# Kernel tuning notes

Hardware: AMD Instinct MI355X
Metric: run time of the kernel (lower is better)

The kernel has to match this reference:

```python
import jax, jax.numpy as jnp
import numpy as np

N0, N1, N2 = 200000, 50000, 10000   # node counts per hop (src -> layer1 targets -> layer2 targets)
E1, E2 = 1000000, 250000
C_IN, H = 128, 256


def setup_inputs() -> dict:
    key = jax.random.key(0)
    ks = jax.random.split(key, 10)
    return {
        "x": jax.random.normal(ks[0], (N0, C_IN), dtype=jnp.float32),
        "src1": jax.random.randint(ks[1], (E1,), 0, N0, dtype=jnp.int32),
        "dst1": jax.random.randint(ks[2], (E1,), 0, N1, dtype=jnp.int32),
        "src2": jax.random.randint(ks[3], (E2,), 0, N1, dtype=jnp.int32),
        "dst2": jax.random.randint(ks[4], (E2,), 0, N2, dtype=jnp.int32),
        "Wl1": jax.random.normal(ks[5], (C_IN, H), dtype=jnp.float32) / np.sqrt(C_IN),
        "Wr1": jax.random.normal(ks[6], (C_IN, H), dtype=jnp.float32) / np.sqrt(C_IN),
        "b1": jnp.zeros((H,), dtype=jnp.float32),
        "Wl2": jax.random.normal(ks[7], (H, H), dtype=jnp.float32) / np.sqrt(H),
        "Wr2": jax.random.normal(ks[8], (H, H), dtype=jnp.float32) / np.sqrt(H),
        "b2": jnp.zeros((H,), dtype=jnp.float32),
    }


def _sage_conv(x_src, x_dst, src, dst, Wl, Wr, b, n_dst):
    # mean aggregation of neighbor messages (PyG SAGEConv, aggr='mean', root_weight=True)
    msgs = x_src[src]                                             # [E, C] irregular gather
    agg = jax.ops.segment_sum(msgs, dst, num_segments=n_dst)      # [n_dst, C]
    cnt = jax.ops.segment_sum(jnp.ones_like(dst, dtype=x_src.dtype), dst, num_segments=n_dst)
    agg = agg / jnp.maximum(cnt, 1.0)[:, None]
    return agg @ Wl + x_dst @ Wr + b


def reference(x, src1, dst1, src2, dst2, Wl1, Wr1, b1, Wl2, Wr2, b2):
    # layer 1: targets are first N1 nodes
    h = _sage_conv(x, x[:N1], src1, dst1, Wl1, Wr1, b1, N1)       # [N1, H]
    h = jax.nn.relu(h)                                            # dropout: eval mode (identity)
    # layer 2: targets are first N2 nodes of the layer-1 output
    out = _sage_conv(h, h[:N2], src2, dst2, Wl2, Wr2, b2, N2)     # [N2, H]
    return out
```

## Files before the change

### kernel.cpp

```cpp
#include <hip/hip_runtime.h>

#define N0 200000
#define N1 50000
#define N2 10000
#define E1 1000000
#define E2 250000
#define CIN 128
#define HD  256

#define SH1   6
#define PK1   18
#define NB1   782
#define CAP1  2048
#define DPB1  64
#define SH2   4
#define PK2   16
#define NB2   625
#define CAP2  640
#define DPB2  16

#define NBIN1 489
#define NBIN2 123
#define NPREP 768
#define NCVT  25000

typedef __attribute__((ext_vector_type(8))) short short8;
typedef __attribute__((ext_vector_type(4))) float f32x4;

__device__ __forceinline__ unsigned short f2bf(float f) {
    unsigned u = __builtin_bit_cast(unsigned, f);
    u = (u + 0x7fffu + ((u >> 16) & 1u)) >> 16;
    return (unsigned short)u;
}
__device__ __forceinline__ float bf2f(unsigned short h) {
    unsigned u = ((unsigned)h) << 16;
    return __builtin_bit_cast(float, u);
}

template<int SHIFTB, int PACKSH, int CAP>
__device__ __forceinline__ void bin_body(
    int bb, const int* __restrict__ src, const int* __restrict__ dst,
    int* __restrict__ gcnt, unsigned* __restrict__ binned, int E, int* sh)
{
    int* hcnt  = sh;
    int* hbase = sh + 1024;
    int* hcur  = sh + 2048;
    const int t = threadIdx.x;
    #pragma unroll
    for (int j = 0; j < 4; j++) hcnt[t + j * 256] = 0;
    __syncthreads();

    unsigned pk[8];
    int      bk[8];
    const int e0 = bb * 2048;
    #pragma unroll
    for (int j = 0; j < 8; j++) {
        const int e = e0 + j * 256 + t;
        if (e < E) {
            const int d = dst[e];
            const int s = src[e];
            bk[j] = d >> SHIFTB;
            pk[j] = ((unsigned)(d & ((1 << SHIFTB) - 1)) << PACKSH) | (unsigned)s;
            atomicAdd(&hcnt[bk[j]], 1);
        } else bk[j] = -1;
    }
    __syncthreads();

    #pragma unroll
    for (int j = 0; j < 4; j++) {
        const int i = t + j * 256;
        hbase[i] = atomicAdd(&gcnt[i], hcnt[i]);
        hcur[i]  = 0;
    }
    __syncthreads();

    #pragma unroll
    for (int j = 0; j < 8; j++) {
        if (bk[j] >= 0) {
            const int idx = atomicAdd(&hcur[bk[j]], 1);
            binned[(size_t)bk[j] * CAP + hbase[bk[j]] + idx] = pk[j];
        }
    }
}

__global__ __launch_bounds__(256) void megaA_kernel(
    const float* __restrict__ x, unsigned short* __restrict__ xb,
    const float* __restrict__ Wl1, const float* __restrict__ Wr1,
    const float* __restrict__ Wl2, const float* __restrict__ Wr2,
    unsigned short* __restrict__ wsw1, unsigned short* __restrict__ wsw2,
    const int* __restrict__ src1, const int* __restrict__ dst1,
    const int* __restrict__ src2, const int* __restrict__ dst2,
    int* __restrict__ gcnt1, int* __restrict__ gcnt2,
    unsigned* __restrict__ binned1, unsigned* __restrict__ binned2)
{
    __shared__ int sh[3072];
    const int b = blockIdx.x;
    const int t = threadIdx.x;

    if (b < NBIN1) {
        bin_body<SH1, PK1, CAP1>(b, src1, dst1, gcnt1, binned1, E1, sh);
    } else if (b < NBIN1 + NBIN2) {
        bin_body<SH2, PK2, CAP2>(b - NBIN1, src2, dst2, gcnt2, binned2, E2, sh);
    } else if (b < NBIN1 + NBIN2 + NPREP) {
        const int pb = b - NBIN1 - NBIN2;
        const float* Wl; const float* Wr; unsigned short* wsw; int K, tid;
        if (pb < 256) { Wl = Wl1; Wr = Wr1; wsw = wsw1; K = CIN; tid = pb * 256 + t; }
        else          { Wl = Wl2; Wr = Wr2; wsw = wsw2; K = HD;  tid = (pb - 256) * 256 + t; }
        const int j  = tid & 7;
        const int L  = (tid >> 3) & 63;
        const int nt = (tid >> 9) & 15;
        const int kt = tid >> 13;
        const int k  = kt * 32 + (L >> 4) * 8 + j;
        const int n  = nt * 16 + (L & 15);
        const float v = (k < K) ? Wl[(size_t)k * HD + n]
                                : Wr[(size_t)(k - K) * HD + n];
        wsw[tid] = f2bf(v);
    } else {
        const int i = (b - NBIN1 - NBIN2 - NPREP) * 256 + t;
        const float4 v = ((const float4*)x)[i];
        ushort4 o;
        o.x = f2bf(v.x); o.y = f2bf(v.y); o.z = f2bf(v.z); o.w = f2bf(v.w);
        ((ushort4*)xb)[i] = o;
    }
}

__global__ __launch_bounds__(512) void layer1_mega(
    const unsigned short* __restrict__ xb,
    const unsigned* __restrict__ binned1, const int* __restrict__ gcnt1,
    const unsigned short* __restrict__ wsw1, const float* __restrict__ bias,
    unsigned short* __restrict__ hb)
{
    __shared__ int ebuf[CAP1];
    __shared__ int lhist[DPB1], loff[DPB1], lcur[DPB1];
    __shared__ __align__(16) unsigned short aggT[4 * DPB1 * 4 * 8];

    const int t = threadIdx.x;
    const int b = blockIdx.x;
    const int cnt = gcnt1[b];
    const unsigned* bp = binned1 + (size_t)b * CAP1;

    if (t < DPB1) lhist[t] = 0;
    __syncthreads();
    for (int i = t; i < cnt; i += 512)
        atomicAdd(&lhist[bp[i] >> PK1], 1);
    __syncthreads();
    const int h0 = (t < DPB1) ? lhist[t] : 0;
    __syncthreads();
    #pragma unroll
    for (int ofs = 1; ofs < DPB1; ofs <<= 1) {
        const int u = (t >= ofs && t < DPB1) ? lhist[t - ofs] : 0;
        __syncthreads();
        if (t < DPB1) lhist[t] += u;
        __syncthreads();
    }
    if (t < DPB1) { loff[t] = lhist[t] - h0; lcur[t] = lhist[t] - h0; }
    __syncthreads();
    for (int i = t; i < cnt; i += 512) {
        const unsigned p = bp[i];
        const int slot = atomicAdd(&lcur[p >> PK1], 1);
        ebuf[slot] = (int)(p & ((1u << PK1) - 1u));
    }
    __syncthreads();

    const int w = t >> 6, L = t & 63, half = L >> 5, l32 = L & 31;
    const int ktw = l32 >> 3, qw = (l32 >> 1) & 3, jo = (l32 & 1) * 4;
    for (int r = w; r < DPB1; r += 8) {
        const int rg = b * DPB1 + r;
        if (rg < N1) {
            const int base = loff[r];
            const int n    = lcur[r] - loff[r];
            float ax = 0.f, ay = 0.f, az = 0.f, aw = 0.f;
            int i = half;
            for (; i + 14 < n; i += 16) {
                ushort4 v[8];
                #pragma unroll
                for (int u = 0; u < 8; u++) {
                    const int s = ebuf[base + i + u * 2];
                    v[u] = *(const ushort4*)(xb + (size_t)s * CIN + l32 * 4);
                }
                #pragma unroll
                for (int u = 0; u < 8; u++) {
                    ax += bf2f(v[u].x); ay += bf2f(v[u].y);
                    az += bf2f(v[u].z); aw += bf2f(v[u].w);
                }
            }
            for (; i < n; i += 2) {
                const int s = ebuf[base + i];
                const ushort4 v = *(const ushort4*)(xb + (size_t)s * CIN + l32 * 4);
                ax += bf2f(v.x); ay += bf2f(v.y); az += bf2f(v.z); aw += bf2f(v.w);
            }
            ax += __shfl_xor(ax, 32);
            ay += __shfl_xor(ay, 32);
            az += __shfl_xor(az, 32);
            aw += __shfl_xor(aw, 32);
            if (half == 0) {
                const float s = 1.0f / fmaxf((float)n, 1.0f);
                ushort4 o;
                o.x = f2bf(ax * s); o.y = f2bf(ay * s);
                o.z = f2bf(az * s); o.w = f2bf(aw * s);
                *(ushort4*)&aggT[(((ktw * DPB1 + r) * 4 + qw) * 8) + jo] = o;
            }
        }
    }
    __syncthreads();

    const int m = L & 15, q = L >> 4;
    const int mt = w & 3, nh = w >> 2;
    const int row_l = mt * 16 + m;
    const int rg2 = min(b * DPB1 + row_l, N1 - 1);
    const unsigned short* a2p = xb + (size_t)rg2 * CIN + q * 8;

    f32x4 acc[8];
    #pragma unroll
    for (int nt = 0; nt < 8; nt++) acc[nt] = (f32x4){0.f, 0.f, 0.f, 0.f};

    #pragma unroll
    for (int kt = 0; kt < 8; kt++) {
        short8 af;
        if (kt < 4) af = *(const short8*)&aggT[((kt * DPB1 + row_l) * 4 + q) * 8];
        else        af = *(const short8*)(a2p + (kt - 4) * 32);
        #pragma unroll
        for (int nt = 0; nt < 8; nt++) {
            const short8 bf = *(const short8*)(
                wsw1 + (((size_t)kt * 16 + (nh * 8 + nt)) * 64 + L) * 8);
            acc[nt] = __builtin_amdgcn_mfma_f32_16x16x32_bf16(af, bf, acc[nt], 0, 0, 0);
        }
    }

    const int orow0 = b * DPB1 + mt * 16 + q * 4;
    #pragma unroll
    for (int nt = 0; nt < 8; nt++) {
        const int col = (nh * 8 + nt) * 16 + m;
        const float bv = bias[col];
        #pragma unroll
        for (int r = 0; r < 4; r++) {
            const int row = orow0 + r;
            if (row < N1) {
                const float v = fmaxf(acc[nt][r] + bv, 0.0f);
                hb[(size_t)row * HD + col] = f2bf(v);
            }
        }
    }
}

__global__ __launch_bounds__(512) void layer2_mega(
    const unsigned short* __restrict__ hb,
    const unsigned* __restrict__ binned2, const int* __restrict__ gcnt2,
    const unsigned short* __restrict__ wsw2, const float* __restrict__ bias,
    float* __restrict__ outp)
{
    __shared__ int ebuf[CAP2];
    __shared__ int lhist[DPB2], loff[DPB2], lcur[DPB2];
    __shared__ __align__(16) unsigned short aggT[8 * DPB2 * 4 * 8];

    const int t = threadIdx.x;
    const int b = blockIdx.x;
    const int cnt = gcnt2[b];
    const unsigned* bp = binned2 + (size_t)b * CAP2;

    if (t < DPB2) lhist[t] = 0;
    __syncthreads();
    for (int i = t; i < cnt; i += 512)
        atomicAdd(&lhist[bp[i] >> PK2], 1);
    __syncthreads();
    const int h0 = (t < DPB2) ? lhist[t] : 0;
    __syncthreads();
    #pragma unroll
    for (int ofs = 1; ofs < DPB2; ofs <<= 1) {
        const int u = (t >= ofs && t < DPB2) ? lhist[t - ofs] : 0;
        __syncthreads();
        if (t < DPB2) lhist[t] += u;
        __syncthreads();
    }
    if (t < DPB2) { loff[t] = lhist[t] - h0; lcur[t] = lhist[t] - h0; }
    __syncthreads();
    for (int i = t; i < cnt; i += 512) {
        const unsigned p = bp[i];
        const int slot = atomicAdd(&lcur[p >> PK2], 1);
        ebuf[slot] = (int)(p & ((1u << PK2) - 1u));
    }
    __syncthreads();

    const int w = t >> 6, L = t & 63;
    const int kt2 = L >> 3, q2 = (L >> 1) & 3, jo2 = (L & 1) * 4;
    for (int r = w; r < DPB2; r += 8) {
        const int base = loff[r];
        const int n    = lcur[r] - loff[r];
        float ax = 0.f, ay = 0.f, az = 0.f, aw = 0.f;
        int i = 0;
        for (; i + 7 < n; i += 8) {
            ushort4 v[8];
            #pragma unroll
            for (int u = 0; u < 8; u++) {
                const int s = ebuf[base + i + u];
                v[u] = *(const ushort4*)(hb + (size_t)s * HD + L * 4);
            }
            #pragma unroll
            for (int u = 0; u < 8; u++) {
                ax += bf2f(v[u].x); ay += bf2f(v[u].y);
                az += bf2f(v[u].z); aw += bf2f(v[u].w);
            }
        }
        for (; i < n; i++) {
            const int s = ebuf[base + i];
            const ushort4 v = *(const ushort4*)(hb + (size_t)s * HD + L * 4);
            ax += bf2f(v.x); ay += bf2f(v.y); az += bf2f(v.z); aw += bf2f(v.w);
        }
        const float s = 1.0f / fmaxf((float)n, 1.0f);
        ushort4 o;
        o.x = f2bf(ax * s); o.y = f2bf(ay * s);
        o.z = f2bf(az * s); o.w = f2bf(aw * s);
        *(ushort4*)&aggT[(((kt2 * DPB2 + r) * 4 + q2) * 8) + jo2] = o;
    }
    __syncthreads();

    const int m = L & 15, q = L >> 4;
    const int rg2 = b * DPB2 + m;
    const unsigned short* a2p = hb + (size_t)rg2 * HD + q * 8;

    f32x4 acc[2];
    acc[0] = (f32x4){0.f, 0.f, 0.f, 0.f};
    acc[1] = (f32x4){0.f, 0.f, 0.f, 0.f};

    #pragma unroll
    for (int kt = 0; kt < 16; kt++) {
        short8 af;
        if (kt < 8) af = *(const short8*)&aggT[((kt * DPB2 + m) * 4 + q) * 8];
        else        af = *(const short8*)(a2p + (kt - 8) * 32);
        #pragma unroll
        for (int nt = 0; nt < 2; nt++) {
            const short8 bf = *(const short8*)(
                wsw2 + (((size_t)kt * 16 + (w * 2 + nt)) * 64 + L) * 8);
            acc[nt] = __builtin_amdgcn_mfma_f32_16x16x32_bf16(af, bf, acc[nt], 0, 0, 0);
        }
    }

    const int orow0 = b * DPB2 + q * 4;
    #pragma unroll
    for (int nt = 0; nt < 2; nt++) {
        const int col = (w * 2 + nt) * 16 + m;
        const float bv = bias[col];
        #pragma unroll
        for (int r = 0; r < 4; r++)
            outp[(size_t)(orow0 + r) * HD + col] = acc[nt][r] + bv;
    }
}

extern "C" void kernel_launch(void* const* d_in, const int* in_sizes, int n_in,
                              void* d_out, int out_size, void* d_ws, size_t ws_size,
                              hipStream_t stream)
{
    const float* x    = (const float*)d_in[0];
    const int*   src1 = (const int*)  d_in[1];
    const int*   dst1 = (const int*)  d_in[2];
    const int*   src2 = (const int*)  d_in[3];
    const int*   dst2 = (const int*)  d_in[4];
    const float* Wl1  = (const float*)d_in[5];
    const float* Wr1  = (const float*)d_in[6];
    const float* b1   = (const float*)d_in[7];
    const float* Wl2  = (const float*)d_in[8];
    const float* Wr2  = (const float*)d_in[9];
    const float* b2   = (const float*)d_in[10];
    float* out = (float*)d_out;

    unsigned short* xb   = (unsigned short*)d_ws;
    unsigned short* hb   = xb + (size_t)N0 * CIN;
    unsigned short* wsw1 = hb + (size_t)N1 * HD;
    unsigned short* wsw2 = wsw1 + 2 * CIN * HD;
    int* gcnt1 = (int*)(wsw2 + 2 * HD * HD);
    int* gcnt2 = gcnt1 + 1024;
    unsigned* binned1 = (unsigned*)(gcnt2 + 1024);
    unsigned* binned2 = binned1 + (size_t)NB1 * CAP1;

    hipMemsetAsync(gcnt1, 0, 2048 * sizeof(int), stream);

    megaA_kernel<<<NBIN1 + NBIN2 + NPREP + NCVT, 256, 0, stream>>>(
        x, xb, Wl1, Wr1, Wl2, Wr2, wsw1, wsw2,
        src1, dst1, src2, dst2, gcnt1, gcnt2, binned1, binned2);

    layer1_mega<<<NB1, 512, 0, stream>>>(xb, binned1, gcnt1, wsw1, b1, hb);
    layer2_mega<<<NB2, 512, 0, stream>>>(hb, binned2, gcnt2, wsw2, b2, out);
}
```

Baseline: 307.3 us.

## Pad neighbor lists to multiples of eight with zero-row sentinel, widen gathers to 16 bytes

```diff
diff --git a/kernel.cpp b/kernel.cpp
--- a/kernel.cpp
+++ b/kernel.cpp
@@ -24,6 +24,9 @@
 #define NPREP 768
 #define NCVT  25000
 
+#define EB1   (CAP1 + 512)
+#define EB2   (CAP2 + 128)
+
 typedef __attribute__((ext_vector_type(8))) short short8;
 typedef __attribute__((ext_vector_type(4))) float f32x4;
 
@@ -85,6 +88,7 @@
 
 __global__ __launch_bounds__(256) void megaA_kernel(
     const float* __restrict__ x, unsigned short* __restrict__ xb,
+    unsigned short* __restrict__ hb,
     const float* __restrict__ Wl1, const float* __restrict__ Wr1,
     const float* __restrict__ Wl2, const float* __restrict__ Wr2,
     unsigned short* __restrict__ wsw1, unsigned short* __restrict__ wsw2,
@@ -115,12 +119,15 @@
         const float v = (k < K) ? Wl[(size_t)k * HD + n]
                                 : Wr[(size_t)(k - K) * HD + n];
         wsw[tid] = f2bf(v);
-    } else {
+    } else if (b < NBIN1 + NBIN2 + NPREP + NCVT) {
         const int i = (b - NBIN1 - NBIN2 - NPREP) * 256 + t;
         const float4 v = ((const float4*)x)[i];
         ushort4 o;
         o.x = f2bf(v.x); o.y = f2bf(v.y); o.z = f2bf(v.z); o.w = f2bf(v.w);
         ((ushort4*)xb)[i] = o;
+    } else {
+        if (t < 64)  ((unsigned*)(xb + (size_t)N0 * CIN))[t] = 0u;
+        if (t < 128) ((unsigned*)(hb + (size_t)N1 * HD))[t]  = 0u;
     }
 }
 
@@ -130,7 +137,7 @@
     const unsigned short* __restrict__ wsw1, const float* __restrict__ bias,
     unsigned short* __restrict__ hb)
 {
-    __shared__ int ebuf[CAP1];
+    __shared__ int ebuf[EB1];
     __shared__ int lhist[DPB1], loff[DPB1], lcur[DPB1];
     __shared__ __align__(16) unsigned short aggT[4 * DPB1 * 4 * 8];
 
@@ -144,16 +151,17 @@
     for (int i = t; i < cnt; i += 512)
         atomicAdd(&lhist[bp[i] >> PK1], 1);
     __syncthreads();
-    const int h0 = (t < DPB1) ? lhist[t] : 0;
-    __syncthreads();
-    #pragma unroll
-    for (int ofs = 1; ofs < DPB1; ofs <<= 1) {
-        const int u = (t >= ofs && t < DPB1) ? lhist[t - ofs] : 0;
-        __syncthreads();
-        if (t < DPB1) lhist[t] += u;
-        __syncthreads();
-    }
-    if (t < DPB1) { loff[t] = lhist[t] - h0; lcur[t] = lhist[t] - h0; }
+    if (t < DPB1) {
+        const int p = (lhist[t] + 7) & ~7;
+        int sum = p;
+        #pragma unroll
+        for (int ofs = 1; ofs < DPB1; ofs <<= 1) {
+            const int u = __shfl_up(sum, ofs);
+            if (t >= ofs) sum += u;
+        }
+        const int st = sum - p;
+        loff[t] = st; lcur[t] = st;
+    }
     __syncthreads();
     for (int i = t; i < cnt; i += 512) {
         const unsigned p = bp[i];
@@ -161,46 +169,46 @@
         ebuf[slot] = (int)(p & ((1u << PK1) - 1u));
     }
     __syncthreads();
-
-    const int w = t >> 6, L = t & 63, half = L >> 5, l32 = L & 31;
-    const int ktw = l32 >> 3, qw = (l32 >> 1) & 3, jo = (l32 & 1) * 4;
-    for (int r = w; r < DPB1; r += 8) {
-        const int rg = b * DPB1 + r;
-        if (rg < N1) {
-            const int base = loff[r];
-            const int n    = lcur[r] - loff[r];
-            float ax = 0.f, ay = 0.f, az = 0.f, aw = 0.f;
-            int i = half;
-            for (; i + 14 < n; i += 16) {
-                ushort4 v[8];
+    if (t < DPB1) {
+        const int h = lhist[t];
+        const int np = (h + 7) & ~7;
+        const int s0 = loff[t];
+        for (int i = s0 + h; i < s0 + np; i++) ebuf[i] = N0;
+    }
+    __syncthreads();
+
+    const int w = t >> 6, L = t & 63;
+    const int qd = L >> 4, l16 = L & 15;
+    const unsigned short* xp = xb + (size_t)l16 * 8;
+    #pragma unroll 1
+    for (int rr = 0; rr < 2; rr++) {
+        const int r = w * 8 + rr * 4 + qd;
+        const int base = loff[r];
+        const int n    = lhist[r];
+        const int npad = (n + 7) & ~7;
+        float acc[8];
+        #pragma unroll
+        for (int j = 0; j < 8; j++) acc[j] = 0.f;
+        for (int i = 0; i < npad; i += 8) {
+            short8 v[8];
+            #pragma unroll
+            for (int u = 0; u < 8; u++) {
+                const int s = ebuf[base + i + u];
+                v[u] = *(const short8*)(xp + (size_t)s * CIN);
+            }
+            #pragma unroll
+            for (int u = 0; u < 8; u++) {
                 #pragma unroll
-                for (int u = 0; u < 8; u++) {
-                    const int s = ebuf[base + i + u * 2];
-                    v[u] = *(const ushort4*)(xb + (size_t)s * CIN + l32 * 4);
-                }
-                #pragma unroll
-                for (int u = 0; u < 8; u++) {
-                    ax += bf2f(v[u].x); ay += bf2f(v[u].y);
-                    az += bf2f(v[u].z); aw += bf2f(v[u].w);
-                }
+                for (int j = 0; j < 8; j++)
+                    acc[j] += bf2f((unsigned short)v[u][j]);
             }
-            for (; i < n; i += 2) {
-                const int s = ebuf[base + i];
-                const ushort4 v = *(const ushort4*)(xb + (size_t)s * CIN + l32 * 4);
-                ax += bf2f(v.x); ay += bf2f(v.y); az += bf2f(v.z); aw += bf2f(v.w);
-            }
-            ax += __shfl_xor(ax, 32);
-            ay += __shfl_xor(ay, 32);
-            az += __shfl_xor(az, 32);
-            aw += __shfl_xor(aw, 32);
-            if (half == 0) {
-                const float s = 1.0f / fmaxf((float)n, 1.0f);
-                ushort4 o;
-                o.x = f2bf(ax * s); o.y = f2bf(ay * s);
-                o.z = f2bf(az * s); o.w = f2bf(aw * s);
-                *(ushort4*)&aggT[(((ktw * DPB1 + r) * 4 + qw) * 8) + jo] = o;
-            }
-        }
+        }
+        const float sc = 1.0f / fmaxf((float)n, 1.0f);
+        short8 o;
+        #pragma unroll
+        for (int j = 0; j < 8; j++) o[j] = (short)f2bf(acc[j] * sc);
+        const int kt = l16 >> 2, q = l16 & 3;
+        *(short8*)&aggT[((kt * DPB1 + r) * 4 + q) * 8] = o;
     }
     __syncthreads();
 
@@ -249,7 +257,7 @@
     const unsigned short* __restrict__ wsw2, const float* __restrict__ bias,
     float* __restrict__ outp)
 {
-    __shared__ int ebuf[CAP2];
+    __shared__ int ebuf[EB2];
     __shared__ int lhist[DPB2], loff[DPB2], lcur[DPB2];
     __shared__ __align__(16) unsigned short aggT[8 * DPB2 * 4 * 8];
 
@@ -263,54 +271,63 @@
     for (int i = t; i < cnt; i += 512)
         atomicAdd(&lhist[bp[i] >> PK2], 1);
     __syncthreads();
-    const int h0 = (t < DPB2) ? lhist[t] : 0;
-    __syncthreads();
-    #pragma unroll
-    for (int ofs = 1; ofs < DPB2; ofs <<= 1) {
-        const int u = (t >= ofs && t < DPB2) ? lhist[t - ofs] : 0;
-        __syncthreads();
-        if (t < DPB2) lhist[t] += u;
-        __syncthreads();
-    }
-    if (t < DPB2) { loff[t] = lhist[t] - h0; lcur[t] = lhist[t] - h0; }
+    if (t < DPB2) {
+        const int p = (lhist[t] + 7) & ~7;
+        int sum = p;
+        #pragma unroll
+        for (int ofs = 1; ofs < DPB2; ofs <<= 1) {
+            const int u = __shfl_up(sum, ofs);
+            if (t >= ofs) sum += u;
+        }
+        const int st = sum - p;
+        loff[t] = st; lcur[t] = st;
+    }
     __syncthreads();
     for (int i = t; i < cnt; i += 512) {
         const unsigned p = bp[i];
         const int slot = atomicAdd(&lcur[p >> PK2], 1);
-        ebuf[slot] = (int)(p & ((1u << PK2) - 1u));
+        ebuf[slot] = (int)(p & 0xFFFFu);
+    }
+    __syncthreads();
+    if (t < DPB2) {
+        const int h = lhist[t];
+        const int np = (h + 7) & ~7;
+        const int s0 = loff[t];
+        for (int i = s0 + h; i < s0 + np; i++) ebuf[i] = N1;
     }
     __syncthreads();
 
     const int w = t >> 6, L = t & 63;
-    const int kt2 = L >> 3, q2 = (L >> 1) & 3, jo2 = (L & 1) * 4;
-    for (int r = w; r < DPB2; r += 8) {
+    const int hf = L >> 5, l32 = L & 31;
+    {
+        const int r = w * 2 + hf;
         const int base = loff[r];
-        const int n    = lcur[r] - loff[r];
-        float ax = 0.f, ay = 0.f, az = 0.f, aw = 0.f;
-        int i = 0;
-        for (; i + 7 < n; i += 8) {
-            ushort4 v[8];
+        const int n    = lhist[r];
+        const int npad = (n + 7) & ~7;
+        float acc[8];
+        #pragma unroll
+        for (int j = 0; j < 8; j++) acc[j] = 0.f;
+        const unsigned short* hp = hb + (size_t)l32 * 8;
+        for (int i = 0; i < npad; i += 8) {
+            short8 v[8];
             #pragma unroll
             for (int u = 0; u < 8; u++) {
                 const int s = ebuf[base + i + u];
-                v[u] = *(const ushort4*)(hb + (size_t)s * HD + L * 4);
+                v[u] = *(const short8*)(hp + (size_t)s * HD);
             }
             #pragma unroll
             for (int u = 0; u < 8; u++) {
-                ax += bf2f(v[u].x); ay += bf2f(v[u].y);
-                az += bf2f(v[u].z); aw += bf2f(v[u].w);
+                #pragma unroll
+                for (int j = 0; j < 8; j++)
+                    acc[j] += bf2f((unsigned short)v[u][j]);
             }
         }
-        for (; i < n; i++) {
-            const int s = ebuf[base + i];
-            const ushort4 v = *(const ushort4*)(hb + (size_t)s * HD + L * 4);
-            ax += bf2f(v.x); ay += bf2f(v.y); az += bf2f(v.z); aw += bf2f(v.w);
-        }
-        const float s = 1.0f / fmaxf((float)n, 1.0f);
-        ushort4 o;
-        o.x = f2bf(ax * s); o.y = f2bf(ay * s);
-        o.z = f2bf(az * s); o.w = f2bf(aw * s);
-        *(ushort4*)&aggT[(((kt2 * DPB2 + r) * 4 + q2) * 8) + jo2] = o;
+        const float sc = 1.0f / fmaxf((float)n, 1.0f);
+        short8 o;
+        #pragma unroll
+        for (int j = 0; j < 8; j++) o[j] = (short)f2bf(acc[j] * sc);
+        const int kt = l32 >> 2, q = l32 & 3;
+        *(short8*)&aggT[((kt * DPB2 + r) * 4 + q) * 8] = o;
     }
     __syncthreads();
 
@@ -364,8 +381,8 @@
     float* out = (float*)d_out;
 
     unsigned short* xb   = (unsigned short*)d_ws;
-    unsigned short* hb   = xb + (size_t)N0 * CIN;
-    unsigned short* wsw1 = hb + (size_t)N1 * HD;
+    unsigned short* hb   = xb + (size_t)(N0 + 1) * CIN;
+    unsigned short* wsw1 = hb + (size_t)(N1 + 1) * HD;
     unsigned short* wsw2 = wsw1 + 2 * CIN * HD;
     int* gcnt1 = (int*)(wsw2 + 2 * HD * HD);
     int* gcnt2 = gcnt1 + 1024;
@@ -374,8 +391,8 @@
 
     hipMemsetAsync(gcnt1, 0, 2048 * sizeof(int), stream);
 
-    megaA_kernel<<<NBIN1 + NBIN2 + NPREP + NCVT, 256, 0, stream>>>(
-        x, xb, Wl1, Wr1, Wl2, Wr2, wsw1, wsw2,
+    megaA_kernel<<<NBIN1 + NBIN2 + NPREP + NCVT + 1, 256, 0, stream>>>(
+        x, xb, hb, Wl1, Wr1, Wl2, Wr2, wsw1, wsw2,
         src1, dst1, src2, dst2, gcnt1, gcnt2, binned1, binned2);
 
     layer1_mega<<<NB1, 512, 0, stream>>>(xb, binned1, gcnt1, wsw1, b1, hb);
```

Measured after the change: 285.9 us. -7.0%, faster.
